# Optimization experiments

Hardware: AMD Instinct MI355X
Metric: run time of the kernel (lower is better)

## Reference

```python
import jax, jax.numpy as jnp
import numpy as np

Q_ZERO = 8  # Q4_0 zero point: w = scale * (q - 8)


def setup_inputs() -> dict:
    key = jax.random.key(0)
    k_x, k_q, k_s, k_b = jax.random.split(key, 4)
    out_f, in_f, block = 11008, 4096, 32
    n_blocks = in_f // block  # 128
    x = jax.random.normal(k_x, (1, 16, in_f), dtype=jnp.float32)
    # 4-bit quantized values per block (0..15), stored as int32 for jax friendliness
    qweight = jax.random.randint(k_q, (out_f, n_blocks, block), 0, 16, dtype=jnp.int32)
    # per-block fp scales (small, like real ggml scales)
    scales = jax.random.uniform(k_s, (out_f, n_blocks), dtype=jnp.float32) * 0.02
    bias = jax.random.normal(k_b, (out_f,), dtype=jnp.float32) * 0.01
    return {"x": x, "qweight": qweight, "scales": scales, "bias": bias}


def reference(x, qweight, scales, bias):
    # ggml_dequantize (Q4_0): w = scale * (q - 8), per block of 32 along infeatures
    out_f, n_blocks, block = qweight.shape
    w = scales[:, :, None] * (qweight.astype(jnp.float32) - Q_ZERO)  # [out, nb, 32]
    w = w.reshape(out_f, n_blocks * block)  # [out, in]
    # x @ W.T + bias, preserving leading dims
    y = jnp.einsum("bsi,oi->bso", x, w) + bias
    return y
```

## Files before the change

### kernel.cpp

```cpp
#include <hip/hip_runtime.h>
#include <stdint.h>


typedef __attribute__((ext_vector_type(8))) short bf16x8;
typedef __attribute__((ext_vector_type(4))) float f32x4;
typedef __attribute__((ext_vector_type(4))) int   i32x4;

#define OUT_F 11008
#define IN_F  4096
#define NB    128

__global__ __launch_bounds__(256) void prep_kernel(const float* __restrict__ x,
                                                   float* __restrict__ out,
                                                   uint32_t* __restrict__ wsA) {
  int tid = blockIdx.x * 256 + threadIdx.x;
  if (tid < 44032) {
    f32x4 z = {0.f, 0.f, 0.f, 0.f};
    ((f32x4*)out)[tid] = z;
  }
  if (tid < 8192) {
    int kb = tid >> 6;
    int l  = tid & 63;
    int t  = l & 15;
    int k  = kb * 32 + (l >> 4) * 8;
    const float* xp = x + t * IN_F + k;
    uint32_t u[8];
#pragma unroll
    for (int j = 0; j < 8; ++j) {
      union { float f; uint32_t i; } c;
      c.f  = xp[j];
      u[j] = c.i + 0x8000u;
    }
    uint4 p;
    p.x = (u[1] & 0xFFFF0000u) | (u[0] >> 16);
    p.y = (u[3] & 0xFFFF0000u) | (u[2] >> 16);
    p.z = (u[5] & 0xFFFF0000u) | (u[4] >> 16);
    p.w = (u[7] & 0xFFFF0000u) | (u[6] >> 16);
    *(uint4*)(wsA + kb * 256 + l * 4) = p;
  }
}

__global__ __launch_bounds__(256) void qgemm_kernel(const int* __restrict__ qw,
                                                    const float* __restrict__ scales,
                                                    const float* __restrict__ bias,
                                                    const uint32_t* __restrict__ wsA,
                                                    float* __restrict__ out) {
  const int bid  = blockIdx.x;
  const int kq   = bid & 3;
  const int ob   = (bid >> 2) << 4;
  const int tid  = threadIdx.x;
  const int wave = tid >> 6;
  const int lane = tid & 63;
  const int col  = lane & 15;
  const int kr   = lane >> 4;

  const int kb0 = kq * 32 + wave * 8;

  const int* qbase = qw + (size_t)(ob + col) * IN_F + kb0 * 32 + kr * 8;
  const uint32_t* abase = wsA + kb0 * 256 + lane * 4;

  const float* sp = scales + (ob + col) * NB + kb0;
  f32x4 sA = *(const f32x4*)sp;
  f32x4 sB = *(const f32x4*)(sp + 4);

  f32x4 acc = {0.f, 0.f, 0.f, 0.f};

#pragma unroll
  for (int i = 0; i < 8; ++i) {
    uint4 a = *(const uint4*)(abase + i * 256);
    const i32x4* qp = (const i32x4*)(qbase + i * 32);
    i32x4 q0 = __builtin_nontemporal_load(qp);
    i32x4 q1 = __builtin_nontemporal_load(qp + 1);
    float s   = (i < 4) ? sA[i] : sB[i - 4];
    float m8s = -8.f * s;
    uint32_t w0 = __float_as_uint(fmaf((float)q0.x, s, m8s));
    uint32_t w1 = __float_as_uint(fmaf((float)q0.y, s, m8s));
    uint32_t w2 = __float_as_uint(fmaf((float)q0.z, s, m8s));
    uint32_t w3 = __float_as_uint(fmaf((float)q0.w, s, m8s));
    uint32_t w4 = __float_as_uint(fmaf((float)q1.x, s, m8s));
    uint32_t w5 = __float_as_uint(fmaf((float)q1.y, s, m8s));
    uint32_t w6 = __float_as_uint(fmaf((float)q1.z, s, m8s));
    uint32_t w7 = __float_as_uint(fmaf((float)q1.w, s, m8s));
    union { uint32_t u[4]; bf16x8 v; } A, B;
    A.u[0] = a.x; A.u[1] = a.y; A.u[2] = a.z; A.u[3] = a.w;
    B.u[0] = __builtin_amdgcn_perm(w1, w0, 0x07060302u);
    B.u[1] = __builtin_amdgcn_perm(w3, w2, 0x07060302u);
    B.u[2] = __builtin_amdgcn_perm(w5, w4, 0x07060302u);
    B.u[3] = __builtin_amdgcn_perm(w7, w6, 0x07060302u);
    acc = __builtin_amdgcn_mfma_f32_16x16x32_bf16(A.v, B.v, acc, 0, 0, 0);
  }

  __shared__ float red[4][256];
#pragma unroll
  for (int r = 0; r < 4; ++r) {
    int t = kr * 4 + r;
    red[wave][t * 16 + col] = acc[r];
  }
  __syncthreads();

  float v = red[0][tid] + red[1][tid] + red[2][tid] + red[3][tid];
  int t = tid >> 4;
  int o = ob + (tid & 15);
  if (kq == 0) v += bias[o];
  __hip_atomic_fetch_add(out + t * OUT_F + o, v, __ATOMIC_RELAXED,
                         __HIP_MEMORY_SCOPE_AGENT);
}

extern "C" void kernel_launch(void* const* d_in, const int* in_sizes, int n_in,
                              void* d_out, int out_size, void* d_ws, size_t ws_size,
                              hipStream_t stream) {
  const float* x      = (const float*)d_in[0];
  const int*   qw     = (const int*)d_in[1];
  const float* scales = (const float*)d_in[2];
  const float* bias   = (const float*)d_in[3];
  float*    out = (float*)d_out;
  uint32_t* wsA = (uint32_t*)d_ws;

  prep_kernel<<<172, 256, 0, stream>>>(x, out, wsA);
  qgemm_kernel<<<2752, 256, 0, stream>>>(qw, scales, bias, wsA, out);
}
```

Before: 256.4 us.

## Fuse activation bf16 conversion into GEMM and drop split-K atomics

Removes the separate prep kernel that zeroed the output and pre-packed activations into bf16. The GEMM now reads fp32 activations directly, converts them in-register, and each block covers the full K range, so results are written with plain stores instead of atomic adds. This saves a kernel launch, the output zeroing and atomic traffic. In exchange the grid shrinks from 2752 to 688 blocks, giving less parallelism for streaming the weights, and activations are converted redundantly in every block.

```diff
diff --git a/kernel.cpp b/kernel.cpp
--- a/kernel.cpp
+++ b/kernel.cpp
@@ -10,84 +10,66 @@
 #define IN_F  4096
 #define NB    128
 
-__global__ __launch_bounds__(256) void prep_kernel(const float* __restrict__ x,
-                                                   float* __restrict__ out,
-                                                   uint32_t* __restrict__ wsA) {
-  int tid = blockIdx.x * 256 + threadIdx.x;
-  if (tid < 44032) {
-    f32x4 z = {0.f, 0.f, 0.f, 0.f};
-    ((f32x4*)out)[tid] = z;
-  }
-  if (tid < 8192) {
-    int kb = tid >> 6;
-    int l  = tid & 63;
-    int t  = l & 15;
-    int k  = kb * 32 + (l >> 4) * 8;
-    const float* xp = x + t * IN_F + k;
-    uint32_t u[8];
-#pragma unroll
-    for (int j = 0; j < 8; ++j) {
-      union { float f; uint32_t i; } c;
-      c.f  = xp[j];
-      u[j] = c.i + 0x8000u;
-    }
-    uint4 p;
-    p.x = (u[1] & 0xFFFF0000u) | (u[0] >> 16);
-    p.y = (u[3] & 0xFFFF0000u) | (u[2] >> 16);
-    p.z = (u[5] & 0xFFFF0000u) | (u[4] >> 16);
-    p.w = (u[7] & 0xFFFF0000u) | (u[6] >> 16);
-    *(uint4*)(wsA + kb * 256 + l * 4) = p;
-  }
-}
-
-__global__ __launch_bounds__(256) void qgemm_kernel(const int* __restrict__ qw,
+__global__ __launch_bounds__(256) void qgemm_kernel(const float* __restrict__ x,
+                                                    const int* __restrict__ qw,
                                                     const float* __restrict__ scales,
                                                     const float* __restrict__ bias,
-                                                    const uint32_t* __restrict__ wsA,
                                                     float* __restrict__ out) {
-  const int bid  = blockIdx.x;
-  const int kq   = bid & 3;
-  const int ob   = (bid >> 2) << 4;
+  const int ob   = blockIdx.x << 4;
   const int tid  = threadIdx.x;
   const int wave = tid >> 6;
   const int lane = tid & 63;
   const int col  = lane & 15;
   const int kr   = lane >> 4;
 
-  const int kb0 = kq * 32 + wave * 8;
+  const int kb0 = wave * 32;
 
-  const int* qbase = qw + (size_t)(ob + col) * IN_F + kb0 * 32 + kr * 8;
-  const uint32_t* abase = wsA + kb0 * 256 + lane * 4;
-
-  const float* sp = scales + (ob + col) * NB + kb0;
-  f32x4 sA = *(const f32x4*)sp;
-  f32x4 sB = *(const f32x4*)(sp + 4);
+  const int*   qbase = qw + (size_t)(ob + col) * IN_F + kb0 * 32 + kr * 8;
+  const float* xbase = x + col * IN_F + kb0 * 32 + kr * 8;
+  const float* sbase = scales + (ob + col) * NB + kb0;
 
   f32x4 acc = {0.f, 0.f, 0.f, 0.f};
 
+  for (int o8 = 0; o8 < 4; ++o8) {
+    f32x4 sA = *(const f32x4*)(sbase + o8 * 8);
+    f32x4 sB = *(const f32x4*)(sbase + o8 * 8 + 4);
 #pragma unroll
-  for (int i = 0; i < 8; ++i) {
-    uint4 a = *(const uint4*)(abase + i * 256);
-    const i32x4* qp = (const i32x4*)(qbase + i * 32);
-    i32x4 q0 = __builtin_nontemporal_load(qp);
-    i32x4 q1 = __builtin_nontemporal_load(qp + 1);
-    float s   = (i < 4) ? sA[i] : sB[i - 4];
-    float m8s = -8.f * s;
-    uint32_t w0 = __float_as_uint(fmaf((float)q0.x, s, m8s));
-    uint32_t w1 = __float_as_uint(fmaf((float)q0.y, s, m8s));
-    uint32_t w2 = __float_as_uint(fmaf((float)q0.z, s, m8s));
-    uint32_t w3 = __float_as_uint(fmaf((float)q0.w, s, m8s));
-    uint32_t w4 = __float_as_uint(fmaf((float)q1.x, s, m8s));
-    uint32_t w5 = __float_as_uint(fmaf((float)q1.y, s, m8s));
-    uint32_t w6 = __float_as_uint(fmaf((float)q1.z, s, m8s));
-    uint32_t w7 = __float_as_uint(fmaf((float)q1.w, s, m8s));
-    union { uint32_t u[4]; bf16x8 v; } A, B;
-    A.u[0] = a.x; A.u[1] = a.y; A.u[2] = a.z; A.u[3] = a.w;
-    B.u[0] = __builtin_amdgcn_perm(w1, w0, 0x07060302u);
-    B.u[1] = __builtin_amdgcn_perm(w3, w2, 0x07060302u);
-    B.u[2] = __builtin_amdgcn_perm(w5, w4, 0x07060302u);
-    B.u[3] = __builtin_amdgcn_perm(w7, w6, 0x07060302u);
-    acc = __builtin_amdgcn_mfma_f32_16x16x32_bf16(A.v, B.v, acc, 0, 0, 0);
+    for (int i = 0; i < 8; ++i) {
+      const int ii = o8 * 8 + i;
+      const i32x4* qp = (const i32x4*)(qbase + ii * 32);
+      i32x4 q0 = __builtin_nontemporal_load(qp);
+      i32x4 q1 = __builtin_nontemporal_load(qp + 1);
+      f32x4 x0 = *(const f32x4*)(xbase + ii * 32);
+      f32x4 x1 = *(const f32x4*)(xbase + ii * 32 + 4);
+      float s   = (i < 4) ? sA[i] : sB[i - 4];
+      float m8s = -8.f * s;
+      union { uint32_t u[4]; bf16x8 v; } A, B;
+      uint32_t a0 = __float_as_uint(x0.x) + 0x8000u;
+      uint32_t a1 = __float_as_uint(x0.y) + 0x8000u;
+      uint32_t a2 = __float_as_uint(x0.z) + 0x8000u;
+      uint32_t a3 = __float_as_uint(x0.w) + 0x8000u;
+      uint32_t a4 = __float_as_uint(x1.x) + 0x8000u;
+      uint32_t a5 = __float_as_uint(x1.y) + 0x8000u;
+      uint32_t a6 = __float_as_uint(x1.z) + 0x8000u;
+      uint32_t a7 = __float_as_uint(x1.w) + 0x8000u;
+      A.u[0] = __builtin_amdgcn_perm(a1, a0, 0x07060302u);
+      A.u[1] = __builtin_amdgcn_perm(a3, a2, 0x07060302u);
+      A.u[2] = __builtin_amdgcn_perm(a5, a4, 0x07060302u);
+      A.u[3] = __builtin_amdgcn_perm(a7, a6, 0x07060302u);
+      uint32_t w0 = __float_as_uint(fmaf((float)q0.x, s, m8s));
+      uint32_t w1 = __float_as_uint(fmaf((float)q0.y, s, m8s));
+      uint32_t w2 = __float_as_uint(fmaf((float)q0.z, s, m8s));
+      uint32_t w3 = __float_as_uint(fmaf((float)q0.w, s, m8s));
+      uint32_t w4 = __float_as_uint(fmaf((float)q1.x, s, m8s));
+      uint32_t w5 = __float_as_uint(fmaf((float)q1.y, s, m8s));
+      uint32_t w6 = __float_as_uint(fmaf((float)q1.z, s, m8s));
+      uint32_t w7 = __float_as_uint(fmaf((float)q1.w, s, m8s));
+      B.u[0] = __builtin_amdgcn_perm(w1, w0, 0x07060302u);
+      B.u[1] = __builtin_amdgcn_perm(w3, w2, 0x07060302u);
+      B.u[2] = __builtin_amdgcn_perm(w5, w4, 0x07060302u);
+      B.u[3] = __builtin_amdgcn_perm(w7, w6, 0x07060302u);
+      acc = __builtin_amdgcn_mfma_f32_16x16x32_bf16(A.v, B.v, acc, 0, 0, 0);
+    }
   }
 
   __shared__ float red[4][256];
@@ -101,9 +83,7 @@
   float v = red[0][tid] + red[1][tid] + red[2][tid] + red[3][tid];
   int t = tid >> 4;
   int o = ob + (tid & 15);
-  if (kq == 0) v += bias[o];
-  __hip_atomic_fetch_add(out + t * OUT_F + o, v, __ATOMIC_RELAXED,
-                         __HIP_MEMORY_SCOPE_AGENT);
+  out[(size_t)t * OUT_F + o] = v + bias[o];
 }
 
 extern "C" void kernel_launch(void* const* d_in, const int* in_sizes, int n_in,
@@ -113,9 +93,7 @@
   const int*   qw     = (const int*)d_in[1];
   const float* scales = (const float*)d_in[2];
   const float* bias   = (const float*)d_in[3];
-  float*    out = (float*)d_out;
-  uint32_t* wsA = (uint32_t*)d_ws;
+  float* out = (float*)d_out;
 
-  prep_kernel<<<172, 256, 0, stream>>>(x, out, wsA);
-  qgemm_kernel<<<2752, 256, 0, stream>>>(qw, scales, bias, wsA, out);
+  qgemm_kernel<<<688, 256, 0, stream>>>(x, qw, scales, bias, out);
 }
```

Result: slower. 267.2 us (+4.2%).
